# Kernel tuning notes

Measured on AMD Instinct MI355X. Metric: run time of the kernel, lower is better.

## Reference

```python
import jax, jax.numpy as jnp
import numpy as np

N, E, CIN = 50000, 400000, 512
GH, GO, TH, HEADS, COUT = 128, 64, 64, 4, 32
BN_EPS = 1e-5


def setup_inputs() -> dict:
    key = jax.random.key(0)
    ks = jax.random.split(key, 40)
    i = iter(range(40))
    nrm = lambda shape, s=0.05: jax.random.normal(ks[next(i)], shape, jnp.float32) * s
    uni = lambda shape, lo, hi: jax.random.uniform(ks[next(i)], shape, jnp.float32, lo, hi)
    inp = {
        'x': jax.random.normal(ks[next(i)], (N, CIN), jnp.float32),
        'edge_index': jax.random.randint(ks[next(i)], (2, E), 0, N, jnp.int32),
        'edge_weight': uni((E,), 0.0, 1.0),
        # GCN layer 1 + BN1 (eval-mode running stats)
        'W1': nrm((CIN, GH)), 'b1': jnp.zeros((GH,), jnp.float32),
        'g1': uni((GH,), 0.9, 1.1), 'be1': nrm((GH,)), 'm1': nrm((GH,)), 'v1': uni((GH,), 0.5, 1.5),
        # GCN layer 2 + BN2
        'W2': nrm((GH, GO)), 'b2': jnp.zeros((GO,), jnp.float32),
        'g2': uni((GO,), 0.9, 1.1), 'be2': nrm((GO,)), 'm2': nrm((GO,)), 'v2': uni((GO,), 0.5, 1.5),
        # TransformerConv (PyG): lin_q/k/v: GO -> HEADS*TH ; skip: GO -> TH
        'Wq': nrm((GO, HEADS * TH)), 'bq': jnp.zeros((HEADS * TH,), jnp.float32),
        'Wk': nrm((GO, HEADS * TH)), 'bk': jnp.zeros((HEADS * TH,), jnp.float32),
        'Wv': nrm((GO, HEADS * TH)), 'bv': jnp.zeros((HEADS * TH,), jnp.float32),
        'Wskip': nrm((GO, TH)), 'bskip': jnp.zeros((TH,), jnp.float32),
        # BN after transformer
        'gt': uni((TH,), 0.9, 1.1), 'bet': nrm((TH,)), 'mt': nrm((TH,)), 'vt': uni((TH,), 0.5, 1.5),
        # final Linear
        'Wfc': nrm((TH, COUT)), 'bfc': jnp.zeros((COUT,), jnp.float32),
    }
    return inp


def _bn_eval(h, g, b, m, v):
    return (h - m) * (g / jnp.sqrt(v + BN_EPS)) + b


def _gcn_conv(x, src, dst, w, W, b):
    # add self loops with weight 1 (PyG gcn_norm default)
    loop = jnp.arange(N, dtype=src.dtype)
    s = jnp.concatenate([src, loop])
    d = jnp.concatenate([dst, loop])
    w2 = jnp.concatenate([w, jnp.ones((N,), x.dtype)])
    deg = jax.ops.segment_sum(w2, d, num_segments=N)
    dinv = jnp.where(deg > 0, jax.lax.rsqrt(deg), 0.0)
    norm = dinv[s] * w2 * dinv[d]                      # [E+N]
    h = x @ W                                          # [N, F]
    out = jax.ops.segment_sum(norm[:, None] * h[s], d, num_segments=N)
    return out + b


def _transformer_conv(x, src, dst, Wq, bq, Wk, bk, Wv, bv, Wskip, bskip):
    # PyG TransformerConv, concat=False (mean over heads), root_weight=True, no self loops
    q = (x @ Wq + bq).reshape(N, HEADS, TH)
    k = (x @ Wk + bk).reshape(N, HEADS, TH)
    v = (x @ Wv + bv).reshape(N, HEADS, TH)
    score = jnp.einsum('ehd,ehd->eh', q[dst], k[src]) / jnp.sqrt(jnp.float32(TH))  # [E,H]
    smax = jax.ops.segment_max(score, dst, num_segments=N)       # [N,H]
    ex = jnp.exp(score - smax[dst])
    denom = jax.ops.segment_sum(ex, dst, num_segments=N)         # [N,H]
    alpha = ex / (denom[dst] + 1e-16)                            # edge softmax over incoming edges
    agg = jax.ops.segment_sum(alpha[:, :, None] * v[src], dst, num_segments=N)  # [N,H,TH]
    out = agg.mean(axis=1)                                       # concat=False -> head mean
    return out + x @ Wskip + bskip


def reference(x, edge_index, edge_weight,
              W1, b1, g1, be1, m1, v1,
              W2, b2, g2, be2, m2, v2,
              Wq, bq, Wk, bk, Wv, bv, Wskip, bskip,
              gt, bet, mt, vt, Wfc, bfc):
    src, dst = edge_index[0], edge_index[1]
    h = _gcn_conv(x, src, dst, edge_weight, W1, b1)
    h = jax.nn.relu(_bn_eval(h, g1, be1, m1, v1))        # dropout = identity in eval
    h = _gcn_conv(h, src, dst, edge_weight, W2, b2)
    z = jax.nn.relu(_bn_eval(h, g2, be2, m2, v2))
    z = _transformer_conv(z, src, dst, Wq, bq, Wk, bk, Wv, bv, Wskip, bskip)
    z = jax.nn.relu(_bn_eval(z, gt, bet, mt, vt))
    return z @ Wfc + bfc
```

## Files before the change

### kernel.cpp

```cpp
#include <hip/hip_runtime.h>
#include <math.h>

namespace {

constexpr int NN = 50000;
constexpr int EE = 400000;
constexpr int CIN = 512;
constexpr int GH = 128;
constexpr int GO = 64;
constexpr int HEADS = 4;
constexpr int COUT = 32;
constexpr float EPS = 1e-5f;
constexpr int PBLK = (NN + 255) / 256;
constexpr int EDGEB = (EE + 255) / 256;
constexpr int PREPB = 128 + (79872 + 255) / 256;
constexpr int GM = (NN + 63) / 64;

typedef __attribute__((ext_vector_type(8))) _Float16 half8;
typedef __attribute__((ext_vector_type(4))) _Float16 half4;
typedef __attribute__((ext_vector_type(2))) _Float16 half2v;
typedef __attribute__((ext_vector_type(4))) float f32x4;

inline int cdiv(int a, int b) { return (a + b - 1) / b; }

__global__ void k_init0(float* deg, int* cnt) {
  int i = blockIdx.x * blockDim.x + threadIdx.x;
  if (i < NN) { deg[i] = 0.0f; cnt[i] = 0; }
}

__device__ __forceinline__ void prep_body(
    int b, int tid,
    const float* __restrict__ Wq, const float* __restrict__ Wk,
    const float* __restrict__ bq, const float* __restrict__ Wv,
    const float* __restrict__ bv, const float* __restrict__ bsk,
    const float* __restrict__ W1, const float* __restrict__ W2,
    const float* __restrict__ Wsk, const float* __restrict__ Wfc,
    _Float16* __restrict__ Mcp, float* __restrict__ cvec,
    _Float16* __restrict__ Bcatp, float* __restrict__ bcomb,
    _Float16* __restrict__ W1p, _Float16* __restrict__ W2p,
    _Float16* __restrict__ Wfcp) {
  if (b < 64) {
    const int i = b, col = tid, h = col >> 6, j = col & 63;
    float acc = 0.f;
    for (int t = 0; t < 64; ++t)
      acc += Wq[i * 256 + h * 64 + t] * Wk[j * 256 + h * 64 + t];
    Mcp[col * 64 + i] = (_Float16)(0.125f * acc);
    if (i == 0) {
      float c = 0.f;
      for (int t = 0; t < 64; ++t) c += bq[h * 64 + t] * Wk[j * 256 + h * 64 + t];
      cvec[col] = 0.125f * c;
    }
  } else if (b < 128) {
    const int idx = (b - 64) * 256 + tid;
    const int rr = idx >> 6, t = idx & 63;
    const int h = rr >> 6, c = rr & 63;
    Bcatp[(size_t)t * 320 + 64 + rr] = (_Float16)(0.25f * Wv[c * 256 + h * 64 + t]);
    if (b == 64 && tid < 64) {
      float s = 0.f;
#pragma unroll
      for (int h2 = 0; h2 < 4; ++h2) s += bv[h2 * 64 + tid];
      bcomb[tid] = bsk[tid] + 0.25f * s;
    }
  } else {
    const int i = (b - 128) * 256 + tid;
    if (i < 65536) { int k = i >> 7, f = i & 127; W1p[f * 512 + k] = (_Float16)W1[i]; }
    else if (i < 73728) { int rel = i - 65536; int k = rel >> 6, f = rel & 63; W2p[f * 128 + k] = (_Float16)W2[rel]; }
    else if (i < 77824) { int rel = i - 73728; int k = rel >> 6, f = rel & 63; Bcatp[f * 320 + k] = (_Float16)Wsk[rel]; }
    else if (i < 79872) { int rel = i - 77824; int k = rel >> 5, f = rel & 31; Wfcp[f * 64 + k] = (_Float16)Wfc[rel]; }
  }
}

__launch_bounds__(256) __global__
void k_edgeprep(const int* __restrict__ ei, const float* __restrict__ w,
                float* __restrict__ deg, int* __restrict__ cnt,
                int* __restrict__ rank,
                const float* __restrict__ Wq, const float* __restrict__ Wk,
                const float* __restrict__ bq, const float* __restrict__ Wv,
                const float* __restrict__ bv, const float* __restrict__ bsk,
                const float* __restrict__ W1, const float* __restrict__ W2,
                const float* __restrict__ Wsk, const float* __restrict__ Wfc,
                _Float16* __restrict__ Mcp, float* __restrict__ cvec,
                _Float16* __restrict__ Bcatp, float* __restrict__ bcomb,
                _Float16* __restrict__ W1p, _Float16* __restrict__ W2p,
                _Float16* __restrict__ Wfcp) {
  if (blockIdx.x < EDGEB) {
    int e = blockIdx.x * 256 + threadIdx.x;
    if (e < EE) {
      int d = ei[EE + e];
      atomicAdd(&deg[d], w[e]);
      rank[e] = atomicAdd(&cnt[d], 1);
    }
  } else {
    prep_body(blockIdx.x - EDGEB, threadIdx.x, Wq, Wk, bq, Wv, bv, bsk,
              W1, W2, Wsk, Wfc, Mcp, cvec, Bcatp, bcomb, W1p, W2p, Wfcp);
  }
}

__global__ void k_node1(const int* __restrict__ cnt, float* __restrict__ dinv,
                        int* __restrict__ part, int* __restrict__ bsum,
                        int* __restrict__ blkhist) {
  __shared__ int wsm[4];
  __shared__ int lh[64];
  const int tid = threadIdx.x, lane = tid & 63, wv = tid >> 6;
  const int i = blockIdx.x * 256 + tid;
  if (tid < 64) lh[tid] = 0;
  __syncthreads();
  int v = (i < NN) ? cnt[i] : 0;
  if (i < NN) {
    dinv[i] = rsqrtf(dinv[i] + 1.0f);
    atomicAdd(&lh[min(v, 63)], 1);
  }
  int x = v;
#pragma unroll
  for (int s = 1; s < 64; s <<= 1) {
    int t = __shfl_up(x, s);
    if (lane >= s) x += t;
  }
  if (lane == 63) wsm[wv] = x;
  __syncthreads();
  if (tid == 0) {
    int r = 0;
#pragma unroll
    for (int j = 0; j < 4; ++j) { int t = wsm[j]; wsm[j] = r; r += t; }
    bsum[blockIdx.x] = r;
  }
  __syncthreads();
  if (i < NN) part[i] = wsm[wv] + x - v;
  if (tid < 64) blkhist[blockIdx.x * 64 + tid] = lh[tid];
}

__launch_bounds__(256) __global__
void k_small(int* __restrict__ bsum, int* __restrict__ ro,
             const int* __restrict__ blkhist, int* __restrict__ blkoff) {
  __shared__ int wsm[4];
  __shared__ int qsum[4][64];
  const int tid = threadIdx.x, lane = tid & 63, wv = tid >> 6;
  {
    int v = (tid < PBLK) ? bsum[tid] : 0;
    int x = v;
#pragma unroll
    for (int s = 1; s < 64; s <<= 1) {
      int t = __shfl_up(x, s);
      if (lane >= s) x += t;
    }
    if (lane == 63) wsm[wv] = x;
    __syncthreads();
    if (tid == 0) {
      int r = 0;
#pragma unroll
      for (int j = 0; j < 4; ++j) { int t = wsm[j]; wsm[j] = r; r += t; }
      ro[NN] = r;
    }
    __syncthreads();
    if (tid < PBLK) bsum[tid] = wsm[wv] + x - v;
  }
  const int c0 = wv * 49, c1 = c0 + 49;
  {
    int qs = 0;
    int k = c0;
    for (; k + 4 <= c1; k += 4) {
      int a = blkhist[(k + 0) * 64 + lane];
      int b = blkhist[(k + 1) * 64 + lane];
      int c = blkhist[(k + 2) * 64 + lane];
      int d = blkhist[(k + 3) * 64 + lane];
      qs += (a + b) + (c + d);
    }
    for (; k < c1; ++k) qs += blkhist[k * 64 + lane];
    qsum[wv][lane] = qs;
  }
  __syncthreads();
  int tot = qsum[0][lane] + qsum[1][lane] + qsum[2][lane] + qsum[3][lane];
  int x = tot;
#pragma unroll
  for (int s = 1; s < 64; s <<= 1) {
    int t = __shfl_up(x, s);
    if (lane >= s) x += t;
  }
  int run = x - tot;
  for (int q = 0; q < wv; ++q) run += qsum[q][lane];
  int k = c0;
  for (; k + 4 <= c1; k += 4) {
    int a = blkhist[(k + 0) * 64 + lane];
    int b = blkhist[(k + 1) * 64 + lane];
    int c = blkhist[(k + 2) * 64 + lane];
    int d = blkhist[(k + 3) * 64 + lane];
    blkoff[(k + 0) * 64 + lane] = run;
    blkoff[(k + 1) * 64 + lane] = run + a;
    blkoff[(k + 2) * 64 + lane] = run + a + b;
    blkoff[(k + 3) * 64 + lane] = run + a + b + c;
    run += (a + b) + (c + d);
  }
  for (; k < c1; ++k) {
    int c = blkhist[k * 64 + lane];
    blkoff[k * 64 + lane] = run;
    run += c;
  }
}

__global__ void k_node2(const int* __restrict__ part, const int* __restrict__ bsum,
                        int* __restrict__ ro, const int* __restrict__ cnt,
                        const int* __restrict__ blkoff, int* __restrict__ perm) {
  __shared__ int lcur[64];
  const int tid = threadIdx.x;
  const int i = blockIdx.x * 256 + tid;
  if (tid < 64) lcur[tid] = 0;
  if (i < NN) ro[i] = part[i] + bsum[i >> 8];
  __syncthreads();
  if (i < NN) {
    int b = min(cnt[i], 63);
    int r = atomicAdd(&lcur[b], 1);
    perm[blkoff[blockIdx.x * 64 + b] + r] = i;
  }
}

template <int F, int K, int LDA, bool AF32, bool OUTF32>
__device__ __forceinline__
void hgemm_body(int bid, const void* __restrict__ Av,
                const _Float16* __restrict__ Bp, const float* __restrict__ bias,
                void* __restrict__ Cv, int M) {
  constexpr int MI = 4;
  constexpr int NR = F / 64;
  constexpr int FW = F / 4;
  constexpr int NT = K / 64;

  __shared__ _Float16 Asm[(AF32 ? 2 : 1) * 64 * 64];
  _Float16* Ah = Asm;
  _Float16* Al = Asm + 64 * 64;

  const int tid = threadIdx.x;
  const int lane = tid & 63;
  const int wc = tid >> 6;
  const int l15 = lane & 15, lhi = lane >> 4;
  const int m0 = bid * 64;
  const int r = tid >> 2, ch = tid & 3;
  const int gr = min(m0 + r, M - 1);

  f32x4 acc[MI][NR];
#pragma unroll
  for (int mi = 0; mi < MI; ++mi)
#pragma unroll
    for (int ni = 0; ni < NR; ++ni) acc[mi][ni] = (f32x4)0.0f;

  float xfA[16], xfB[16];
  half8 xhA0, xhA1, xhB0, xhB1;

  auto LOADA = [&](int kk) {
    if constexpr (AF32) {
      const float4* src = reinterpret_cast<const float4*>(
          (const float*)Av + (size_t)gr * LDA + kk + ch * 16);
      float4 f0 = src[0], f1 = src[1], f2 = src[2], f3 = src[3];
      xfA[0] = f0.x; xfA[1] = f0.y; xfA[2] = f0.z; xfA[3] = f0.w;
      xfA[4] = f1.x; xfA[5] = f1.y; xfA[6] = f1.z; xfA[7] = f1.w;
      xfA[8] = f2.x; xfA[9] = f2.y; xfA[10] = f2.z; xfA[11] = f2.w;
      xfA[12] = f3.x; xfA[13] = f3.y; xfA[14] = f3.z; xfA[15] = f3.w;
    } else {
      const half8* src = reinterpret_cast<const half8*>(
          (const _Float16*)Av + (size_t)gr * LDA + kk + ch * 16);
      xhA0 = src[0];
      xhA1 = src[1];
    }
  };
  auto LOADB = [&](int kk) {
    if constexpr (AF32) {
      const float4* src = reinterpret_cast<const float4*>(
          (const float*)Av + (size_t)gr * LDA + kk + ch * 16);
      float4 f0 = src[0], f1 = src[1], f2 = src[2], f3 = src[3];
      xfB[0] = f0.x; xfB[1] = f0.y; xfB[2] = f0.z; xfB[3] = f0.w;
      xfB[4] = f1.x; xfB[5] = f1.y; xfB[6] = f1.z; xfB[7] = f1.w;
      xfB[8] = f2.x; xfB[9] = f2.y; xfB[10] = f2.z; xfB[11] = f2.w;
      xfB[12] = f3.x; xfB[13] = f3.y; xfB[14] = f3.z; xfB[15] = f3.w;
    } else {
      const half8* src = reinterpret_cast<const half8*>(
          (const _Float16*)Av + (size_t)gr * LDA + kk + ch * 16);
      xhB0 = src[0];
      xhB1 = src[1];
    }
  };

  const int sbase = r * 128 + ch * 32;
  const int ssw = (r & 7) << 4;
  auto STOREA = [&]() {
    if constexpr (AF32) {
      half8 vh0, vl0, vh1, vl1;
#pragma unroll
      for (int i = 0; i < 8; ++i) {
        _Float16 h = (_Float16)xfA[i];
        vh0[i] = h; vl0[i] = (_Float16)(xfA[i] - (float)h);
      }
#pragma unroll
      for (int i = 0; i < 8; ++i) {
        _Float16 h = (_Float16)xfA[8 + i];
        vh1[i] = h; vl1[i] = (_Float16)(xfA[8 + i] - (float)h);
      }
      *reinterpret_cast<half8*>((char*)Ah + (sbase ^ ssw)) = vh0;
      *reinterpret_cast<half8*>((char*)Ah + ((sbase + 16) ^ ssw)) = vh1;
      *reinterpret_cast<half8*>((char*)Al + (sbase ^ ssw)) = vl0;
      *reinterpret_cast<half8*>((char*)Al + ((sbase + 16) ^ ssw)) = vl1;
    } else {
      *reinterpret_cast<half8*>((char*)Ah + (sbase ^ ssw)) = xhA0;
      *reinterpret_cast<half8*>((char*)Ah + ((sbase + 16) ^ ssw)) = xhA1;
    }
  };
  auto STOREB = [&]() {
    if constexpr (AF32) {
      half8 vh0, vl0, vh1, vl1;
#pragma unroll
      for (int i = 0; i < 8; ++i) {
        _Float16 h = (_Float16)xfB[i];
        vh0[i] = h; vl0[i] = (_Float16)(xfB[i] - (float)h);
      }
#pragma unroll
      for (int i = 0; i < 8; ++i) {
        _Float16 h = (_Float16)xfB[8 + i];
        vh1[i] = h; vl1[i] = (_Float16)(xfB[8 + i] - (float)h);
      }
      *reinterpret_cast<half8*>((char*)Ah + (sbase ^ ssw)) = vh0;
      *reinterpret_cast<half8*>((char*)Ah + ((sbase + 16) ^ ssw)) = vh1;
      *reinterpret_cast<half8*>((char*)Al + (sbase ^ ssw)) = vl0;
      *reinterpret_cast<half8*>((char*)Al + ((sbase + 16) ^ ssw)) = vl1;
    } else {
      *reinterpret_cast<half8*>((char*)Ah + (sbase ^ ssw)) = xhB0;
      *reinterpret_cast<half8*>((char*)Ah + ((sbase + 16) ^ ssw)) = xhB1;
    }
  };

  LOADA(0);
  if constexpr (NT > 1) LOADB(64);

#pragma unroll
  for (int t = 0; t < NT; ++t) {
    if ((t & 1) == 0) STOREA(); else STOREB();
    __syncthreads();
    if ((t & 1) == 0) {
      if (t + 2 < NT) LOADA((t + 2) * 64);
    } else {
      if (t + 2 < NT) LOADB((t + 2) * 64);
    }
    const int k0 = t * 64;
#pragma unroll
    for (int ks = 0; ks < 2; ++ks) {
      half8 ah[MI], al[MI];
#pragma unroll
      for (int mi = 0; mi < MI; ++mi) {
        const int row = mi * 16 + l15;
        const int off = (row * 128 + (ks * 32 + lhi * 8) * 2) ^ ((row & 7) << 4);
        ah[mi] = *reinterpret_cast<const half8*>((const char*)Ah + off);
        if constexpr (AF32)
          al[mi] = *reinterpret_cast<const half8*>((const char*)Al + off);
      }
#pragma unroll
      for (int ni = 0; ni < NR; ++ni) {
        const int col = wc * FW + ni * 16 + l15;
        const half8 bf = *reinterpret_cast<const half8*>(
            Bp + (size_t)col * K + k0 + ks * 32 + lhi * 8);
#pragma unroll
        for (int mi = 0; mi < MI; ++mi) {
          acc[mi][ni] = __builtin_amdgcn_mfma_f32_16x16x32_f16(ah[mi], bf, acc[mi][ni], 0, 0, 0);
          if constexpr (AF32)
            acc[mi][ni] = __builtin_amdgcn_mfma_f32_16x16x32_f16(al[mi], bf, acc[mi][ni], 0, 0, 0);
        }
      }
    }
    __syncthreads();
  }

#pragma unroll
  for (int ni = 0; ni < NR; ++ni) {
    const int col = wc * FW + ni * 16 + l15;
    const float bvv = bias ? bias[col] : 0.0f;
#pragma unroll
    for (int mi = 0; mi < MI; ++mi) {
#pragma unroll
      for (int rr = 0; rr < 4; ++rr) {
        const int orow = m0 + mi * 16 + lhi * 4 + rr;
        if (orow < M) {
          float val = acc[mi][ni][rr] + bvv;
          if (OUTF32)
            ((float*)Cv)[(size_t)orow * F + col] = val;
          else
            ((_Float16*)Cv)[(size_t)orow * F + col] = (_Float16)val;
        }
      }
    }
  }
}

template <int F, int K, int LDA, bool AF32, bool OUTF32>
__launch_bounds__(256) __global__
void hgemm(const void* __restrict__ Av, const _Float16* __restrict__ Bp,
           const float* __restrict__ bias, void* __restrict__ Cv, int M) {
  hgemm_body<F, K, LDA, AF32, OUTF32>(blockIdx.x, Av, Bp, bias, Cv, M);
}

__launch_bounds__(256) __global__
void k_fillgemm1(const int* __restrict__ ei, const float* __restrict__ w,
                 const float* __restrict__ dinv, const int* __restrict__ ro,
                 const int* __restrict__ rank, int* __restrict__ csr_src,
                 float* __restrict__ csr_nrm, const float* __restrict__ x,
                 const _Float16* __restrict__ W1p, _Float16* __restrict__ h1f,
                 int M) {
  if (blockIdx.x < GM) {
    hgemm_body<128, 512, 512, true, false>(blockIdx.x, x, W1p, nullptr, h1f, M);
  } else {
    int e = (blockIdx.x - GM) * 256 + threadIdx.x;
    if (e < EE) {
      int s = ei[e], d = ei[EE + e];
      int p = ro[d] + rank[e];
      csr_src[p] = s;
      csr_nrm[p] = dinv[s] * w[e] * dinv[d];
    }
  }
}

__launch_bounds__(256) __global__
void k_aggfc(const _Float16* __restrict__ zu, const _Float16* __restrict__ Bcatp,
             const float* __restrict__ bcomb, const _Float16* __restrict__ Wfcp,
             const float* __restrict__ bfc, float* __restrict__ out, int M,
             const float* __restrict__ gt, const float* __restrict__ bet,
             const float* __restrict__ mt, const float* __restrict__ vt) {
  __shared__ _Float16 Ah[64 * 64];
  __shared__ _Float16 Gs[64 * 64];

  const int tid = threadIdx.x;
  const int lane = tid & 63;
  const int wid = tid >> 6;
  const int l15 = lane & 15, lhi = lane >> 4;
  const int m0 = blockIdx.x * 64;
  const int r = tid >> 2, ch = tid & 3;
  const int gr = min(m0 + r, M - 1);

  f32x4 acc[4];
#pragma unroll
  for (int mi = 0; mi < 4; ++mi) acc[mi] = (f32x4)0.0f;

  half8 xhA0, xhA1, xhB0, xhB1;
  auto LOADA = [&](int kk) {
    const half8* src = reinterpret_cast<const half8*>(
        zu + (size_t)gr * 320 + kk + ch * 16);
    xhA0 = src[0]; xhA1 = src[1];
  };
  auto LOADB = [&](int kk) {
    const half8* src = reinterpret_cast<const half8*>(
        zu + (size_t)gr * 320 + kk + ch * 16);
    xhB0 = src[0]; xhB1 = src[1];
  };
  const int sbase = r * 128 + ch * 32;
  const int ssw = (r & 7) << 4;
  auto STOREA = [&]() {
    *reinterpret_cast<half8*>((char*)Ah + (sbase ^ ssw)) = xhA0;
    *reinterpret_cast<half8*>((char*)Ah + ((sbase + 16) ^ ssw)) = xhA1;
  };
  auto STOREB = [&]() {
    *reinterpret_cast<half8*>((char*)Ah + (sbase ^ ssw)) = xhB0;
    *reinterpret_cast<half8*>((char*)Ah + ((sbase + 16) ^ ssw)) = xhB1;
  };

  LOADA(0);
  LOADB(64);
#pragma unroll
  for (int t = 0; t < 5; ++t) {
    if ((t & 1) == 0) STOREA(); else STOREB();
    __syncthreads();
    if ((t & 1) == 0) {
      if (t + 2 < 5) LOADA((t + 2) * 64);
    } else {
      if (t + 2 < 5) LOADB((t + 2) * 64);
    }
    const int k0 = t * 64;
#pragma unroll
    for (int ks = 0; ks < 2; ++ks) {
      half8 ah[4];
#pragma unroll
      for (int mi = 0; mi < 4; ++mi) {
        const int row = mi * 16 + l15;
        const int off = (row * 128 + (ks * 32 + lhi * 8) * 2) ^ ((row & 7) << 4);
        ah[mi] = *reinterpret_cast<const half8*>((const char*)Ah + off);
      }
      const int col = wid * 16 + l15;
      const half8 bf = *reinterpret_cast<const half8*>(
          Bcatp + (size_t)col * 320 + k0 + ks * 32 + lhi * 8);
#pragma unroll
      for (int mi = 0; mi < 4; ++mi)
        acc[mi] = __builtin_amdgcn_mfma_f32_16x16x32_f16(ah[mi], bf, acc[mi], 0, 0, 0);
    }
    __syncthreads();
  }

  {
    const int col = wid * 16 + l15;
    const float bns = gt[col] * rsqrtf(vt[col] + EPS);
    const float bnb = bet[col], bnm = mt[col], bco = bcomb[col];
#pragma unroll
    for (int mi = 0; mi < 4; ++mi) {
#pragma unroll
      for (int rr = 0; rr < 4; ++rr) {
        const int row = mi * 16 + lhi * 4 + rr;
        float val = acc[mi][rr] + bco;
        val = (val - bnm) * bns + bnb;
        val = val > 0.f ? val : 0.f;
        const int boff = (row * 128 + col * 2) ^ ((row & 7) << 4);
        *reinterpret_cast<_Float16*>((char*)Gs + boff) = (_Float16)val;
      }
    }
  }
  __syncthreads();

  f32x4 acc2[2];
#pragma unroll
  for (int ni = 0; ni < 2; ++ni) acc2[ni] = (f32x4)0.0f;
#pragma unroll
  for (int ks = 0; ks < 2; ++ks) {
    const int row = wid * 16 + l15;
    const int off = (row * 128 + (ks * 32 + lhi * 8) * 2) ^ ((row & 7) << 4);
    const half8 ag = *reinterpret_cast<const half8*>((const char*)Gs + off);
#pragma unroll
    for (int ni = 0; ni < 2; ++ni) {
      const int col = ni * 16 + l15;
      const half8 bf = *reinterpret_cast<const half8*>(
          Wfcp + (size_t)col * 64 + ks * 32 + lhi * 8);
      acc2[ni] = __builtin_amdgcn_mfma_f32_16x16x32_f16(ag, bf, acc2[ni], 0, 0, 0);
    }
  }
#pragma unroll
  for (int ni = 0; ni < 2; ++ni) {
    const int col = ni * 16 + l15;
#pragma unroll
    for (int rr = 0; rr < 4; ++rr) {
      const int orow = m0 + wid * 16 + lhi * 4 + rr;
      if (orow < M) out[(size_t)orow * COUT + col] = acc2[ni][rr] + bfc[col];
    }
  }
}

__launch_bounds__(256) __global__
void k_gcn128(const int* __restrict__ ro, const int* __restrict__ csr_src,
              const float* __restrict__ csr_nrm, const int* __restrict__ perm,
              const _Float16* __restrict__ h, const float* __restrict__ dinv,
              const float* __restrict__ bias, const float* __restrict__ g,
              const float* __restrict__ be, const float* __restrict__ m,
              const float* __restrict__ v, _Float16* __restrict__ out) {
  const int idx = blockIdx.x * 4 + (threadIdx.x >> 6);
  const int lane = threadIdx.x & 63;
  if (idx >= NN) return;
  const int wid = perm[idx];
  const float di = dinv[wid];
  const float di2 = di * di;
  const int p0 = ro[wid], p1 = ro[wid + 1];

  half2v sv = *reinterpret_cast<const half2v*>(h + (size_t)wid * 128 + lane * 2);
  float2 a[4];
  a[0] = make_float2((float)sv[0] * di2, (float)sv[1] * di2);
  a[1] = make_float2(0.f, 0.f);
  a[2] = make_float2(0.f, 0.f);
  a[3] = make_float2(0.f, 0.f);
  int p = p0;
  for (; p + 8 <= p1; p += 8) {
    int s[8]; float w[8];
#pragma unroll
    for (int j = 0; j < 8; ++j) { s[j] = csr_src[p + j]; w[j] = csr_nrm[p + j]; }
    half2v hv[8];
#pragma unroll
    for (int j = 0; j < 8; ++j)
      hv[j] = *reinterpret_cast<const half2v*>(h + (size_t)s[j] * 128 + lane * 2);
#pragma unroll
    for (int j = 0; j < 8; ++j) {
      a[j & 3].x += w[j] * (float)hv[j][0];
      a[j & 3].y += w[j] * (float)hv[j][1];
    }
  }
  for (; p + 4 <= p1; p += 4) {
    int s[4]; float w[4];
#pragma unroll
    for (int j = 0; j < 4; ++j) { s[j] = csr_src[p + j]; w[j] = csr_nrm[p + j]; }
    half2v hv[4];
#pragma unroll
    for (int j = 0; j < 4; ++j)
      hv[j] = *reinterpret_cast<const half2v*>(h + (size_t)s[j] * 128 + lane * 2);
#pragma unroll
    for (int j = 0; j < 4; ++j) {
      a[j].x += w[j] * (float)hv[j][0];
      a[j].y += w[j] * (float)hv[j][1];
    }
  }
  for (; p < p1; ++p) {
    int s = csr_src[p];
    float w = csr_nrm[p];
    half2v hv = *reinterpret_cast<const half2v*>(h + (size_t)s * 128 + lane * 2);
    a[1].x += w * (float)hv[0]; a[1].y += w * (float)hv[1];
  }
  float ax = (a[0].x + a[1].x) + (a[2].x + a[3].x);
  float ay = (a[0].y + a[1].y) + (a[2].y + a[3].y);
  float2 gg = reinterpret_cast<const float2*>(g)[lane];
  float2 bb = reinterpret_cast<const float2*>(be)[lane];
  float2 mm = reinterpret_cast<const float2*>(m)[lane];
  float2 vv = reinterpret_cast<const float2*>(v)[lane];
  float2 bi = reinterpret_cast<const float2*>(bias)[lane];
  float s0 = gg.x * rsqrtf(vv.x + EPS);
  float s1 = gg.y * rsqrtf(vv.y + EPS);
  float y0 = (ax + bi.x - mm.x) * s0 + bb.x;
  float y1 = (ay + bi.y - mm.y) * s1 + bb.y;
  half2v o;
  o[0] = (_Float16)(y0 > 0.f ? y0 : 0.f);
  o[1] = (_Float16)(y1 > 0.f ? y1 : 0.f);
  *reinterpret_cast<half2v*>(out + (size_t)wid * 128 + lane * 2) = o;
}

__launch_bounds__(256) __global__
void k_gcn64(const int* __restrict__ ro, const int* __restrict__ csr_src,
             const float* __restrict__ csr_nrm, const int* __restrict__ perm,
             const _Float16* __restrict__ h, const float* __restrict__ dinv,
             const float* __restrict__ bias, const float* __restrict__ g,
             const float* __restrict__ be, const float* __restrict__ m,
             const float* __restrict__ v, _Float16* __restrict__ zu) {
  const int idx = blockIdx.x * 4 + (threadIdx.x >> 6);
  const int lane = threadIdx.x & 63;
  if (idx >= NN) return;
  const int wid = perm[idx];
  const float di = dinv[wid];
  const float di2 = di * di;
  const int p0 = ro[wid], p1 = ro[wid + 1];

  float a[4];
  a[0] = (float)h[(size_t)wid * 64 + lane] * di2;
  a[1] = 0.f; a[2] = 0.f; a[3] = 0.f;
  int p = p0;
  for (; p + 8 <= p1; p += 8) {
    int s[8]; float w[8];
#pragma unroll
    for (int j = 0; j < 8; ++j) { s[j] = csr_src[p + j]; w[j] = csr_nrm[p + j]; }
    float hv[8];
#pragma unroll
    for (int j = 0; j < 8; ++j) hv[j] = (float)h[(size_t)s[j] * 64 + lane];
#pragma unroll
    for (int j = 0; j < 8; ++j) a[j & 3] += w[j] * hv[j];
  }
  for (; p + 4 <= p1; p += 4) {
    int s[4]; float w[4];
#pragma unroll
    for (int j = 0; j < 4; ++j) { s[j] = csr_src[p + j]; w[j] = csr_nrm[p + j]; }
    float hv[4];
#pragma unroll
    for (int j = 0; j < 4; ++j) hv[j] = (float)h[(size_t)s[j] * 64 + lane];
#pragma unroll
    for (int j = 0; j < 4; ++j) a[j] += w[j] * hv[j];
  }
  for (; p < p1; ++p) a[1] += csr_nrm[p] * (float)h[(size_t)csr_src[p] * 64 + lane];
  float av = (a[0] + a[1]) + (a[2] + a[3]);
  float sc = g[lane] * rsqrtf(v[lane] + EPS);
  float y = (av + bias[lane] - m[lane]) * sc + be[lane];
  zu[(size_t)wid * 320 + lane] = (_Float16)(y > 0.f ? y : 0.f);
}

__launch_bounds__(256) __global__
void k_attn(const int* __restrict__ ro, const int* __restrict__ csr_src,
            const int* __restrict__ perm, _Float16* zu,
            const _Float16* __restrict__ qpp) {
  const int wave = blockIdx.x * 4 + (threadIdx.x >> 6);
  const int lane = threadIdx.x & 63;
  const int g = lane >> 4;
  const int t = lane & 15;
  const bool bit3 = (t & 8) != 0, bit2 = (t & 4) != 0;

  const int idx = wave * 4 + g;
  const bool valid = idx < NN;
  const int dst = perm[valid ? idx : 0];

  float4 q[4];
#pragma unroll
  for (int h = 0; h < 4; ++h) {
    half4 qh = *reinterpret_cast<const half4*>(qpp + (size_t)dst * 256 + h * 64 + t * 4);
    q[h] = make_float4((float)qh[0], (float)qh[1], (float)qh[2], (float)qh[3]);
  }

  float4 ua[4];
  float den[4];
#pragma unroll
  for (int h = 0; h < 4; ++h) {
    ua[h] = make_float4(0.f, 0.f, 0.f, 0.f);
    den[h] = 0.f;
  }

  int p = valid ? ro[dst] : 0;
  const int pend = valid ? ro[dst + 1] : 0;

  auto reduce4 = [&](float pa0, float pa1, float pa2, float pa3,
                     float& o0, float& o1, float& o2, float& o3) {
    float send1 = bit3 ? pa0 : pa2;
    float recv1 = __shfl_xor(send1, 8);
    float a0 = (bit3 ? pa2 : pa0) + recv1;
    float send2 = bit3 ? pa1 : pa3;
    float recv2 = __shfl_xor(send2, 8);
    float a1 = (bit3 ? pa3 : pa1) + recv2;
    float send3 = bit2 ? a0 : a1;
    float recv3 = __shfl_xor(send3, 4);
    float b = (bit2 ? a1 : a0) + recv3;
    b += __shfl_xor(b, 2);
    b += __shfl_xor(b, 1);
    float r4 = __shfl_xor(b, 4);
    float r8 = __shfl_xor(b, 8);
    float r84 = __shfl_xor(r4, 8);
    o0 = bit3 ? (bit2 ? r84 : r8) : (bit2 ? r4 : b);
    o1 = bit3 ? (bit2 ? r8 : r84) : (bit2 ? b : r4);
    o2 = bit3 ? (bit2 ? r4 : b) : (bit2 ? r84 : r8);
    o3 = bit3 ? (bit2 ? b : r4) : (bit2 ? r8 : r84);
  };

  int sA = csr_src[min(p, EE - 1)];
  int sB = csr_src[min(p + 1, EE - 1)];
  half4 znA = *reinterpret_cast<const half4*>(zu + (size_t)sA * 320 + t * 4);
  half4 znB = *reinterpret_cast<const half4*>(zu + (size_t)sB * 320 + t * 4);

  while (__ballot(p < pend)) {
    const bool actA = p < pend;
    const bool actB = (p + 1) < pend;
    const float4 zvA = make_float4((float)znA[0], (float)znA[1], (float)znA[2], (float)znA[3]);
    const float4 zvB = make_float4((float)znB[0], (float)znB[1], (float)znB[2], (float)znB[3]);
    sA = csr_src[min(p + 2, EE - 1)];
    sB = csr_src[min(p + 3, EE - 1)];
    znA = *reinterpret_cast<const half4*>(zu + (size_t)sA * 320 + t * 4);
    znB = *reinterpret_cast<const half4*>(zu + (size_t)sB * 320 + t * 4);

    float pA0 = q[0].x * zvA.x + q[0].y * zvA.y + q[0].z * zvA.z + q[0].w * zvA.w;
    float pA1 = q[1].x * zvA.x + q[1].y * zvA.y + q[1].z * zvA.z + q[1].w * zvA.w;
    float pA2 = q[2].x * zvA.x + q[2].y * zvA.y + q[2].z * zvA.z + q[2].w * zvA.w;
    float pA3 = q[3].x * zvA.x + q[3].y * zvA.y + q[3].z * zvA.z + q[3].w * zvA.w;
    float pB0 = q[0].x * zvB.x + q[0].y * zvB.y + q[0].z * zvB.z + q[0].w * zvB.w;
    float pB1 = q[1].x * zvB.x + q[1].y * zvB.y + q[1].z * zvB.z + q[1].w * zvB.w;
    float pB2 = q[2].x * zvB.x + q[2].y * zvB.y + q[2].z * zvB.z + q[2].w * zvB.w;
    float pB3 = q[3].x * zvB.x + q[3].y * zvB.y + q[3].z * zvB.z + q[3].w * zvB.w;

    float sA0, sA1, sA2, sA3, sB0, sB1, sB2, sB3;
    reduce4(pA0, pA1, pA2, pA3, sA0, sA1, sA2, sA3);
    reduce4(pB0, pB1, pB2, pB3, sB0, sB1, sB2, sB3);

    float eA0 = actA ? __expf(fminf(sA0, 60.f)) : 0.f;
    float eA1 = actA ? __expf(fminf(sA1, 60.f)) : 0.f;
    float eA2 = actA ? __expf(fminf(sA2, 60.f)) : 0.f;
    float eA3 = actA ? __expf(fminf(sA3, 60.f)) : 0.f;
    float eB0 = actB ? __expf(fminf(sB0, 60.f)) : 0.f;
    float eB1 = actB ? __expf(fminf(sB1, 60.f)) : 0.f;
    float eB2 = actB ? __expf(fminf(sB2, 60.f)) : 0.f;
    float eB3 = actB ? __expf(fminf(sB3, 60.f)) : 0.f;

    den[0] += eA0 + eB0; den[1] += eA1 + eB1;
    den[2] += eA2 + eB2; den[3] += eA3 + eB3;
    ua[0].x += eA0 * zvA.x + eB0 * zvB.x; ua[0].y += eA0 * zvA.y + eB0 * zvB.y;
    ua[0].z += eA0 * zvA.z + eB0 * zvB.z; ua[0].w += eA0 * zvA.w + eB0 * zvB.w;
    ua[1].x += eA1 * zvA.x + eB1 * zvB.x; ua[1].y += eA1 * zvA.y + eB1 * zvB.y;
    ua[1].z += eA1 * zvA.z + eB1 * zvB.z; ua[1].w += eA1 * zvA.w + eB1 * zvB.w;
    ua[2].x += eA2 * zvA.x + eB2 * zvB.x; ua[2].y += eA2 * zvA.y + eB2 * zvB.y;
    ua[2].z += eA2 * zvA.z + eB2 * zvB.z; ua[2].w += eA2 * zvA.w + eB2 * zvB.w;
    ua[3].x += eA3 * zvA.x + eB3 * zvB.x; ua[3].y += eA3 * zvA.y + eB3 * zvB.y;
    ua[3].z += eA3 * zvA.z + eB3 * zvB.z; ua[3].w += eA3 * zvA.w + eB3 * zvB.w;
    p += 2;
  }

  if (valid) {
#pragma unroll
    for (int h = 0; h < 4; ++h) {
      float inv = 1.0f / (den[h] + 1e-16f);
      half4 o;
      o[0] = (_Float16)(ua[h].x * inv);
      o[1] = (_Float16)(ua[h].y * inv);
      o[2] = (_Float16)(ua[h].z * inv);
      o[3] = (_Float16)(ua[h].w * inv);
      *reinterpret_cast<half4*>(zu + (size_t)dst * 320 + 64 + h * 64 + t * 4) = o;
    }
  }
}

}

extern "C" void kernel_launch(void* const* d_in, const int* in_sizes, int n_in,
                              void* d_out, int out_size, void* d_ws, size_t ws_size,
                              hipStream_t stream) {
  const float* x   = (const float*)d_in[0];
  const int*   ei  = (const int*)d_in[1];
  const float* ew  = (const float*)d_in[2];
  const float* W1  = (const float*)d_in[3];
  const float* b1  = (const float*)d_in[4];
  const float* g1  = (const float*)d_in[5];
  const float* be1 = (const float*)d_in[6];
  const float* m1  = (const float*)d_in[7];
  const float* v1  = (const float*)d_in[8];
  const float* W2  = (const float*)d_in[9];
  const float* b2  = (const float*)d_in[10];
  const float* g2  = (const float*)d_in[11];
  const float* be2 = (const float*)d_in[12];
  const float* m2  = (const float*)d_in[13];
  const float* v2  = (const float*)d_in[14];
  const float* Wq  = (const float*)d_in[15];
  const float* bq  = (const float*)d_in[16];
  const float* Wk  = (const float*)d_in[17];
  const float* Wv  = (const float*)d_in[19];
  const float* bv  = (const float*)d_in[20];
  const float* Wsk = (const float*)d_in[21];
  const float* bsk = (const float*)d_in[22];
  const float* gt  = (const float*)d_in[23];
  const float* bet = (const float*)d_in[24];
  const float* mt  = (const float*)d_in[25];
  const float* vt  = (const float*)d_in[26];
  const float* Wfc = (const float*)d_in[27];
  const float* bfc = (const float*)d_in[28];

  constexpr int NP = 50048;
  float* ws = (float*)d_ws;
  float* dinv    = ws;
  int*   cnt     = (int*)(dinv + NP);
  int*   rank    = cnt + NP;
  int*   ro      = rank + EE;
  int*   perm    = ro + NP;
  int*   part    = perm + NP;
  int*   bsum    = part + NP;
  int*   csr_src = bsum + 256;
  float* csr_nrm = (float*)(csr_src + EE);
  int*   blkhist = (int*)(csr_nrm + EE);
  int*   blkoff  = blkhist + PBLK * 64;
  float* cvec    = (float*)(blkoff + PBLK * 64 + 64);
  float* bcomb   = cvec + 256;
  _Float16* Mcp   = (_Float16*)(bcomb + 64);
  _Float16* Bcatp = Mcp + 256 * 64;
  _Float16* W1p   = Bcatp + 64 * 320;
  _Float16* W2p   = W1p + 128 * 512;
  _Float16* Wfcp  = W2p + 64 * 128;
  _Float16* h1f   = Wfcp + 32 * 64;
  _Float16* a1f   = h1f + (size_t)NP * 128;
  _Float16* h2f   = a1f + (size_t)NP * 128;
  _Float16* zuf   = h2f + (size_t)NP * 64;
  _Float16* qppf  = zuf + (size_t)NP * 320;

  const int tb = 256;

  k_init0<<<cdiv(NN, tb), tb, 0, stream>>>(dinv, cnt);
  k_edgeprep<<<EDGEB + PREPB, 256, 0, stream>>>(
      ei, ew, dinv, cnt, rank, Wq, Wk, bq, Wv, bv, bsk, W1, W2, Wsk, Wfc,
      Mcp, cvec, Bcatp, bcomb, W1p, W2p, Wfcp);
  k_node1<<<PBLK, 256, 0, stream>>>(cnt, dinv, part, bsum, blkhist);
  k_small<<<1, 256, 0, stream>>>(bsum, ro, blkhist, blkoff);
  k_node2<<<PBLK, 256, 0, stream>>>(part, bsum, ro, cnt, blkoff, perm);

  k_fillgemm1<<<GM + EDGEB, 256, 0, stream>>>(ei, ew, dinv, ro, rank, csr_src,
                                              csr_nrm, x, W1p, h1f, NN);

  k_gcn128<<<cdiv(NN, 4), 256, 0, stream>>>(ro, csr_src, csr_nrm, perm, h1f, dinv,
                                            b1, g1, be1, m1, v1, a1f);
  hgemm<64, 128, 128, false, false><<<GM, 256, 0, stream>>>(a1f, W2p, nullptr, h2f, NN);
  k_gcn64<<<cdiv(NN, 4), 256, 0, stream>>>(ro, csr_src, csr_nrm, perm, h2f, dinv,
                                           b2, g2, be2, m2, v2, zuf);

  hgemm<256, 64, 320, false, false><<<GM, 256, 0, stream>>>(zuf, Mcp, cvec, qppf, NN);
  k_attn<<<cdiv(NN, 16), 256, 0, stream>>>(ro, csr_src, perm, zuf, qppf);

  k_aggfc<<<GM, 256, 0, stream>>>(zuf, Bcatp, bcomb, Wfcp, bfc, (float*)d_out, NN,
                                  gt, bet, mt, vt);
}
```

Measured before the change: 228.5 us.

## Pre-convert x to fp16 and drop split-precision GEMM1; pack CSR src/norm

Adds a conversion pass in the edge-prep kernel that writes x as fp16. The first GEMM can then use single-pass fp16 MFMA instead of hi/lo split-fp16 emulation, which halves its MFMA count and its LDS traffic. Separately, the CSR source index and normalisation weight are packed into one int2 array, so the gather kernels issue one load per edge instead of two. The trade-off is an extra read and write of x (about 150 MB of traffic), lower precision on the first layer's input, and more bytes read in the attention kernel, which only needs the index.

```diff
diff --git a/kernel.cpp b/kernel.cpp
--- a/kernel.cpp
+++ b/kernel.cpp
@@ -13,6 +13,7 @@
 constexpr float EPS = 1e-5f;
 constexpr int PBLK = (NN + 255) / 256;
 constexpr int EDGEB = (EE + 255) / 256;
+constexpr int CVTB = (NN * CIN) / 2048;
 constexpr int PREPB = 128 + (79872 + 255) / 256;
 constexpr int GM = (NN + 63) / 64;
 
@@ -73,7 +74,8 @@
 __launch_bounds__(256) __global__
 void k_edgeprep(const int* __restrict__ ei, const float* __restrict__ w,
                 float* __restrict__ deg, int* __restrict__ cnt,
-                int* __restrict__ rank,
+                int* __restrict__ rank, const float* __restrict__ x,
+                _Float16* __restrict__ x16,
                 const float* __restrict__ Wq, const float* __restrict__ Wk,
                 const float* __restrict__ bq, const float* __restrict__ Wv,
                 const float* __restrict__ bv, const float* __restrict__ bsk,
@@ -90,8 +92,18 @@
       atomicAdd(&deg[d], w[e]);
       rank[e] = atomicAdd(&cnt[d], 1);
     }
+  } else if (blockIdx.x < EDGEB + CVTB) {
+    const int base = (blockIdx.x - EDGEB) * 2048 + threadIdx.x * 8;
+    const float4 f0 = *reinterpret_cast<const float4*>(x + base);
+    const float4 f1 = *reinterpret_cast<const float4*>(x + base + 4);
+    half8 o;
+    o[0] = (_Float16)f0.x; o[1] = (_Float16)f0.y;
+    o[2] = (_Float16)f0.z; o[3] = (_Float16)f0.w;
+    o[4] = (_Float16)f1.x; o[5] = (_Float16)f1.y;
+    o[6] = (_Float16)f1.z; o[7] = (_Float16)f1.w;
+    *reinterpret_cast<half8*>(x16 + base) = o;
   } else {
-    prep_body(blockIdx.x - EDGEB, threadIdx.x, Wq, Wk, bq, Wv, bv, bsk,
+    prep_body(blockIdx.x - EDGEB - CVTB, threadIdx.x, Wq, Wk, bq, Wv, bv, bsk,
               W1, W2, Wsk, Wfc, Mcp, cvec, Bcatp, bcomb, W1p, W2p, Wfcp);
   }
 }
@@ -213,9 +225,9 @@
   }
 }
 
-template <int F, int K, int LDA, bool AF32, bool OUTF32>
+template <int F, int K, int LDA, bool OUTF32>
 __device__ __forceinline__
-void hgemm_body(int bid, const void* __restrict__ Av,
+void hgemm_body(int bid, const _Float16* __restrict__ Av,
                 const _Float16* __restrict__ Bp, const float* __restrict__ bias,
                 void* __restrict__ Cv, int M) {
   constexpr int MI = 4;
@@ -223,9 +235,7 @@
   constexpr int FW = F / 4;
   constexpr int NT = K / 64;
 
-  __shared__ _Float16 Asm[(AF32 ? 2 : 1) * 64 * 64];
-  _Float16* Ah = Asm;
-  _Float16* Al = Asm + 64 * 64;
+  __shared__ _Float16 Ah[64 * 64];
 
   const int tid = threadIdx.x;
   const int lane = tid & 63;
@@ -241,87 +251,26 @@
 #pragma unroll
     for (int ni = 0; ni < NR; ++ni) acc[mi][ni] = (f32x4)0.0f;
 
-  float xfA[16], xfB[16];
   half8 xhA0, xhA1, xhB0, xhB1;
-
   auto LOADA = [&](int kk) {
-    if constexpr (AF32) {
-      const float4* src = reinterpret_cast<const float4*>(
-          (const float*)Av + (size_t)gr * LDA + kk + ch * 16);
-      float4 f0 = src[0], f1 = src[1], f2 = src[2], f3 = src[3];
-      xfA[0] = f0.x; xfA[1] = f0.y; xfA[2] = f0.z; xfA[3] = f0.w;
-      xfA[4] = f1.x; xfA[5] = f1.y; xfA[6] = f1.z; xfA[7] = f1.w;
-      xfA[8] = f2.x; xfA[9] = f2.y; xfA[10] = f2.z; xfA[11] = f2.w;
-      xfA[12] = f3.x; xfA[13] = f3.y; xfA[14] = f3.z; xfA[15] = f3.w;
-    } else {
-      const half8* src = reinterpret_cast<const half8*>(
-          (const _Float16*)Av + (size_t)gr * LDA + kk + ch * 16);
-      xhA0 = src[0];
-      xhA1 = src[1];
-    }
+    const half8* src = reinterpret_cast<const half8*>(
+        Av + (size_t)gr * LDA + kk + ch * 16);
+    xhA0 = src[0]; xhA1 = src[1];
   };
   auto LOADB = [&](int kk) {
-    if constexpr (AF32) {
-      const float4* src = reinterpret_cast<const float4*>(
-          (const float*)Av + (size_t)gr * LDA + kk + ch * 16);
-      float4 f0 = src[0], f1 = src[1], f2 = src[2], f3 = src[3];
-      xfB[0] = f0.x; xfB[1] = f0.y; xfB[2] = f0.z; xfB[3] = f0.w;
-      xfB[4] = f1.x; xfB[5] = f1.y; xfB[6] = f1.z; xfB[7] = f1.w;
-      xfB[8] = f2.x; xfB[9] = f2.y; xfB[10] = f2.z; xfB[11] = f2.w;
-      xfB[12] = f3.x; xfB[13] = f3.y; xfB[14] = f3.z; xfB[15] = f3.w;
-    } else {
-      const half8* src = reinterpret_cast<const half8*>(
-          (const _Float16*)Av + (size_t)gr * LDA + kk + ch * 16);
-      xhB0 = src[0];
-      xhB1 = src[1];
-    }
+    const half8* src = reinterpret_cast<const half8*>(
+        Av + (size_t)gr * LDA + kk + ch * 16);
+    xhB0 = src[0]; xhB1 = src[1];
   };
-
   const int sbase = r * 128 + ch * 32;
   const int ssw = (r & 7) << 4;
   auto STOREA = [&]() {
-    if constexpr (AF32) {
-      half8 vh0, vl0, vh1, vl1;
-#pragma unroll
-      for (int i = 0; i < 8; ++i) {
-        _Float16 h = (_Float16)xfA[i];
-        vh0[i] = h; vl0[i] = (_Float16)(xfA[i] - (float)h);
-      }
-#pragma unroll
-      for (int i = 0; i < 8; ++i) {
-        _Float16 h = (_Float16)xfA[8 + i];
-        vh1[i] = h; vl1[i] = (_Float16)(xfA[8 + i] - (float)h);
-      }
-      *reinterpret_cast<half8*>((char*)Ah + (sbase ^ ssw)) = vh0;
-      *reinterpret_cast<half8*>((char*)Ah + ((sbase + 16) ^ ssw)) = vh1;
-      *reinterpret_cast<half8*>((char*)Al + (sbase ^ ssw)) = vl0;
-      *reinterpret_cast<half8*>((char*)Al + ((sbase + 16) ^ ssw)) = vl1;
-    } else {
-      *reinterpret_cast<half8*>((char*)Ah + (sbase ^ ssw)) = xhA0;
-      *reinterpret_cast<half8*>((char*)Ah + ((sbase + 16) ^ ssw)) = xhA1;
-    }
+    *reinterpret_cast<half8*>((char*)Ah + (sbase ^ ssw)) = xhA0;
+    *reinterpret_cast<half8*>((char*)Ah + ((sbase + 16) ^ ssw)) = xhA1;
   };
   auto STOREB = [&]() {
-    if constexpr (AF32) {
-      half8 vh0, vl0, vh1, vl1;
-#pragma unroll
-      for (int i = 0; i < 8; ++i) {
-        _Float16 h = (_Float16)xfB[i];
-        vh0[i] = h; vl0[i] = (_Float16)(xfB[i] - (float)h);
-      }
-#pragma unroll
-      for (int i = 0; i < 8; ++i) {
-        _Float16 h = (_Float16)xfB[8 + i];
-        vh1[i] = h; vl1[i] = (_Float16)(xfB[8 + i] - (float)h);
-      }
-      *reinterpret_cast<half8*>((char*)Ah + (sbase ^ ssw)) = vh0;
-      *reinterpret_cast<half8*>((char*)Ah + ((sbase + 16) ^ ssw)) = vh1;
-      *reinterpret_cast<half8*>((char*)Al + (sbase ^ ssw)) = vl0;
-      *reinterpret_cast<half8*>((char*)Al + ((sbase + 16) ^ ssw)) = vl1;
-    } else {
-      *reinterpret_cast<half8*>((char*)Ah + (sbase ^ ssw)) = xhB0;
-      *reinterpret_cast<half8*>((char*)Ah + ((sbase + 16) ^ ssw)) = xhB1;
-    }
+    *reinterpret_cast<half8*>((char*)Ah + (sbase ^ ssw)) = xhB0;
+    *reinterpret_cast<half8*>((char*)Ah + ((sbase + 16) ^ ssw)) = xhB1;
   };
 
   LOADA(0);
@@ -339,14 +288,12 @@
     const int k0 = t * 64;
 #pragma unroll
     for (int ks = 0; ks < 2; ++ks) {
-      half8 ah[MI], al[MI];
+      half8 ah[MI];
 #pragma unroll
       for (int mi = 0; mi < MI; ++mi) {
         const int row = mi * 16 + l15;
         const int off = (row * 128 + (ks * 32 + lhi * 8) * 2) ^ ((row & 7) << 4);
         ah[mi] = *reinterpret_cast<const half8*>((const char*)Ah + off);
-        if constexpr (AF32)
-          al[mi] = *reinterpret_cast<const half8*>((const char*)Al + off);
       }
 #pragma unroll
       for (int ni = 0; ni < NR; ++ni) {
@@ -354,11 +301,8 @@
         const half8 bf = *reinterpret_cast<const half8*>(
             Bp + (size_t)col * K + k0 + ks * 32 + lhi * 8);
 #pragma unroll
-        for (int mi = 0; mi < MI; ++mi) {
+        for (int mi = 0; mi < MI; ++mi)
           acc[mi][ni] = __builtin_amdgcn_mfma_f32_16x16x32_f16(ah[mi], bf, acc[mi][ni], 0, 0, 0);
-          if constexpr (AF32)
-            acc[mi][ni] = __builtin_amdgcn_mfma_f32_16x16x32_f16(al[mi], bf, acc[mi][ni], 0, 0, 0);
-        }
       }
     }
     __syncthreads();
@@ -385,29 +329,31 @@
   }
 }
 
-template <int F, int K, int LDA, bool AF32, bool OUTF32>
+template <int F, int K, int LDA, bool OUTF32>
 __launch_bounds__(256) __global__
-void hgemm(const void* __restrict__ Av, const _Float16* __restrict__ Bp,
+void hgemm(const _Float16* __restrict__ Av, const _Float16* __restrict__ Bp,
            const float* __restrict__ bias, void* __restrict__ Cv, int M) {
-  hgemm_body<F, K, LDA, AF32, OUTF32>(blockIdx.x, Av, Bp, bias, Cv, M);
+  hgemm_body<F, K, LDA, OUTF32>(blockIdx.x, Av, Bp, bias, Cv, M);
 }
 
 __launch_bounds__(256) __global__
 void k_fillgemm1(const int* __restrict__ ei, const float* __restrict__ w,
                  const float* __restrict__ dinv, const int* __restrict__ ro,
-                 const int* __restrict__ rank, int* __restrict__ csr_src,
-                 float* __restrict__ csr_nrm, const float* __restrict__ x,
+                 const int* __restrict__ rank, int2* __restrict__ csrp,
+                 const _Float16* __restrict__ x16,
                  const _Float16* __restrict__ W1p, _Float16* __restrict__ h1f,
                  int M) {
   if (blockIdx.x < GM) {
-    hgemm_body<128, 512, 512, true, false>(blockIdx.x, x, W1p, nullptr, h1f, M);
+    hgemm_body<128, 512, 512, false>(blockIdx.x, x16, W1p, nullptr, h1f, M);
   } else {
     int e = (blockIdx.x - GM) * 256 + threadIdx.x;
     if (e < EE) {
       int s = ei[e], d = ei[EE + e];
       int p = ro[d] + rank[e];
-      csr_src[p] = s;
-      csr_nrm[p] = dinv[s] * w[e] * dinv[d];
+      int2 pk;
+      pk.x = s;
+      pk.y = __float_as_int(dinv[s] * w[e] * dinv[d]);
+      csrp[p] = pk;
     }
   }
 }
@@ -533,8 +479,8 @@
 }
 
 __launch_bounds__(256) __global__
-void k_gcn128(const int* __restrict__ ro, const int* __restrict__ csr_src,
-              const float* __restrict__ csr_nrm, const int* __restrict__ perm,
+void k_gcn128(const int* __restrict__ ro, const int2* __restrict__ csrp,
+              const int* __restrict__ perm,
               const _Float16* __restrict__ h, const float* __restrict__ dinv,
               const float* __restrict__ bias, const float* __restrict__ g,
               const float* __restrict__ be, const float* __restrict__ m,
@@ -555,37 +501,39 @@
   a[3] = make_float2(0.f, 0.f);
   int p = p0;
   for (; p + 8 <= p1; p += 8) {
-    int s[8]; float w[8];
-#pragma unroll
-    for (int j = 0; j < 8; ++j) { s[j] = csr_src[p + j]; w[j] = csr_nrm[p + j]; }
+    int2 pk[8];
+#pragma unroll
+    for (int j = 0; j < 8; ++j) pk[j] = csrp[p + j];
     half2v hv[8];
 #pragma unroll
     for (int j = 0; j < 8; ++j)
-      hv[j] = *reinterpret_cast<const half2v*>(h + (size_t)s[j] * 128 + lane * 2);
+      hv[j] = *reinterpret_cast<const half2v*>(h + (size_t)pk[j].x * 128 + lane * 2);
 #pragma unroll
     for (int j = 0; j < 8; ++j) {
-      a[j & 3].x += w[j] * (float)hv[j][0];
-      a[j & 3].y += w[j] * (float)hv[j][1];
+      float w = __int_as_float(pk[j].y);
+      a[j & 3].x += w * (float)hv[j][0];
+      a[j & 3].y += w * (float)hv[j][1];
     }
   }
   for (; p + 4 <= p1; p += 4) {
-    int s[4]; float w[4];
-#pragma unroll
-    for (int j = 0; j < 4; ++j) { s[j] = csr_src[p + j]; w[j] = csr_nrm[p + j]; }
+    int2 pk[4];
+#pragma unroll
+    for (int j = 0; j < 4; ++j) pk[j] = csrp[p + j];
     half2v hv[4];
 #pragma unroll
     for (int j = 0; j < 4; ++j)
-      hv[j] = *reinterpret_cast<const half2v*>(h + (size_t)s[j] * 128 + lane * 2);
+      hv[j] = *reinterpret_cast<const half2v*>(h + (size_t)pk[j].x * 128 + lane * 2);
 #pragma unroll
     for (int j = 0; j < 4; ++j) {
-      a[j].x += w[j] * (float)hv[j][0];
-      a[j].y += w[j] * (float)hv[j][1];
+      float w = __int_as_float(pk[j].y);
+      a[j].x += w * (float)hv[j][0];
+      a[j].y += w * (float)hv[j][1];
     }
   }
   for (; p < p1; ++p) {
-    int s = csr_src[p];
-    float w = csr_nrm[p];
-    half2v hv = *reinterpret_cast<const half2v*>(h + (size_t)s * 128 + lane * 2);
+    int2 pk = csrp[p];
+    float w = __int_as_float(pk.y);
+    half2v hv = *reinterpret_cast<const half2v*>(h + (size_t)pk.x * 128 + lane * 2);
     a[1].x += w * (float)hv[0]; a[1].y += w * (float)hv[1];
   }
   float ax = (a[0].x + a[1].x) + (a[2].x + a[3].x);
@@ -606,8 +554,8 @@
 }
 
 __launch_bounds__(256) __global__
-void k_gcn64(const int* __restrict__ ro, const int* __restrict__ csr_src,
-             const float* __restrict__ csr_nrm, const int* __restrict__ perm,
+void k_gcn64(const int* __restrict__ ro, const int2* __restrict__ csrp,
+             const int* __restrict__ perm,
              const _Float16* __restrict__ h, const float* __restrict__ dinv,
              const float* __restrict__ bias, const float* __restrict__ g,
              const float* __restrict__ be, const float* __restrict__ m,
@@ -625,26 +573,29 @@
   a[1] = 0.f; a[2] = 0.f; a[3] = 0.f;
   int p = p0;
   for (; p + 8 <= p1; p += 8) {
-    int s[8]; float w[8];
-#pragma unroll
-    for (int j = 0; j < 8; ++j) { s[j] = csr_src[p + j]; w[j] = csr_nrm[p + j]; }
+    int2 pk[8];
+#pragma unroll
+    for (int j = 0; j < 8; ++j) pk[j] = csrp[p + j];
     float hv[8];
 #pragma unroll
-    for (int j = 0; j < 8; ++j) hv[j] = (float)h[(size_t)s[j] * 64 + lane];
-#pragma unroll
-    for (int j = 0; j < 8; ++j) a[j & 3] += w[j] * hv[j];
+    for (int j = 0; j < 8; ++j) hv[j] = (float)h[(size_t)pk[j].x * 64 + lane];
+#pragma unroll
+    for (int j = 0; j < 8; ++j) a[j & 3] += __int_as_float(pk[j].y) * hv[j];
   }
   for (; p + 4 <= p1; p += 4) {
-    int s[4]; float w[4];
-#pragma unroll
-    for (int j = 0; j < 4; ++j) { s[j] = csr_src[p + j]; w[j] = csr_nrm[p + j]; }
+    int2 pk[4];
+#pragma unroll
+    for (int j = 0; j < 4; ++j) pk[j] = csrp[p + j];
     float hv[4];
 #pragma unroll
-    for (int j = 0; j < 4; ++j) hv[j] = (float)h[(size_t)s[j] * 64 + lane];
-#pragma unroll
-    for (int j = 0; j < 4; ++j) a[j] += w[j] * hv[j];
-  }
-  for (; p < p1; ++p) a[1] += csr_nrm[p] * (float)h[(size_t)csr_src[p] * 64 + lane];
+    for (int j = 0; j < 4; ++j) hv[j] = (float)h[(size_t)pk[j].x * 64 + lane];
+#pragma unroll
+    for (int j = 0; j < 4; ++j) a[j] += __int_as_float(pk[j].y) * hv[j];
+  }
+  for (; p < p1; ++p) {
+    int2 pk = csrp[p];
+    a[1] += __int_as_float(pk.y) * (float)h[(size_t)pk.x * 64 + lane];
+  }
   float av = (a[0] + a[1]) + (a[2] + a[3]);
   float sc = g[lane] * rsqrtf(v[lane] + EPS);
   float y = (av + bias[lane] - m[lane]) * sc + be[lane];
@@ -652,7 +603,7 @@
 }
 
 __launch_bounds__(256) __global__
-void k_attn(const int* __restrict__ ro, const int* __restrict__ csr_src,
+void k_attn(const int* __restrict__ ro, const int2* __restrict__ csrp,
             const int* __restrict__ perm, _Float16* zu,
             const _Float16* __restrict__ qpp) {
   const int wave = blockIdx.x * 4 + (threadIdx.x >> 6);
@@ -705,8 +656,8 @@
     o3 = bit3 ? (bit2 ? b : r4) : (bit2 ? r8 : r84);
   };
 
-  int sA = csr_src[min(p, EE - 1)];
-  int sB = csr_src[min(p + 1, EE - 1)];
+  int sA = csrp[min(p, EE - 1)].x;
+  int sB = csrp[min(p + 1, EE - 1)].x;
   half4 znA = *reinterpret_cast<const half4*>(zu + (size_t)sA * 320 + t * 4);
   half4 znB = *reinterpret_cast<const half4*>(zu + (size_t)sB * 320 + t * 4);
 
@@ -715,8 +666,8 @@
     const bool actB = (p + 1) < pend;
     const float4 zvA = make_float4((float)znA[0], (float)znA[1], (float)znA[2], (float)znA[3]);
     const float4 zvB = make_float4((float)znB[0], (float)znB[1], (float)znB[2], (float)znB[3]);
-    sA = csr_src[min(p + 2, EE - 1)];
-    sB = csr_src[min(p + 3, EE - 1)];
+    sA = csrp[min(p + 2, EE - 1)].x;
+    sB = csrp[min(p + 3, EE - 1)].x;
     znA = *reinterpret_cast<const half4*>(zu + (size_t)sA * 320 + t * 4);
     znB = *reinterpret_cast<const half4*>(zu + (size_t)sB * 320 + t * 4);
 
@@ -812,9 +763,8 @@
   int*   perm    = ro + NP;
   int*   part    = perm + NP;
   int*   bsum    = part + NP;
-  int*   csr_src = bsum + 256;
-  float* csr_nrm = (float*)(csr_src + EE);
-  int*   blkhist = (int*)(csr_nrm + EE);
+  int2*  csrp    = (int2*)(bsum + 256);
+  int*   blkhist = (int*)(csrp + EE);
   int*   blkoff  = blkhist + PBLK * 64;
   float* cvec    = (float*)(blkoff + PBLK * 64 + 64);
   float* bcomb   = cvec + 256;
@@ -823,7 +773,8 @@
   _Float16* W1p   = Bcatp + 64 * 320;
   _Float16* W2p   = W1p + 128 * 512;
   _Float16* Wfcp  = W2p + 64 * 128;
-  _Float16* h1f   = Wfcp + 32 * 64;
+  _Float16* x16   = Wfcp + 32 * 64;
+  _Float16* h1f   = x16 + (size_t)NP * 512;
   _Float16* a1f   = h1f + (size_t)NP * 128;
   _Float16* h2f   = a1f + (size_t)NP * 128;
   _Float16* zuf   = h2f + (size_t)NP * 64;
@@ -832,24 +783,24 @@
   const int tb = 256;
 
   k_init0<<<cdiv(NN, tb), tb, 0, stream>>>(dinv, cnt);
-  k_edgeprep<<<EDGEB + PREPB, 256, 0, stream>>>(
-      ei, ew, dinv, cnt, rank, Wq, Wk, bq, Wv, bv, bsk, W1, W2, Wsk, Wfc,
+  k_edgeprep<<<EDGEB + CVTB + PREPB, 256, 0, stream>>>(
+      ei, ew, dinv, cnt, rank, x, x16, Wq, Wk, bq, Wv, bv, bsk, W1, W2, Wsk, Wfc,
       Mcp, cvec, Bcatp, bcomb, W1p, W2p, Wfcp);
   k_node1<<<PBLK, 256, 0, stream>>>(cnt, dinv, part, bsum, blkhist);
   k_small<<<1, 256, 0, stream>>>(bsum, ro, blkhist, blkoff);
   k_node2<<<PBLK, 256, 0, stream>>>(part, bsum, ro, cnt, blkoff, perm);
 
-  k_fillgemm1<<<GM + EDGEB, 256, 0, stream>>>(ei, ew, dinv, ro, rank, csr_src,
-                                              csr_nrm, x, W1p, h1f, NN);
-
-  k_gcn128<<<cdiv(NN, 4), 256, 0, stream>>>(ro, csr_src, csr_nrm, perm, h1f, dinv,
+  k_fillgemm1<<<GM + EDGEB, 256, 0, stream>>>(ei, ew, dinv, ro, rank, csrp,
+                                              x16, W1p, h1f, NN);
+
+  k_gcn128<<<cdiv(NN, 4), 256, 0, stream>>>(ro, csrp, perm, h1f, dinv,
                                             b1, g1, be1, m1, v1, a1f);
-  hgemm<64, 128, 128, false, false><<<GM, 256, 0, stream>>>(a1f, W2p, nullptr, h2f, NN);
-  k_gcn64<<<cdiv(NN, 4), 256, 0, stream>>>(ro, csr_src, csr_nrm, perm, h2f, dinv,
+  hgemm<64, 128, 128, false><<<GM, 256, 0, stream>>>(a1f, W2p, nullptr, h2f, NN);
+  k_gcn64<<<cdiv(NN, 4), 256, 0, stream>>>(ro, csrp, perm, h2f, dinv,
                                            b2, g2, be2, m2, v2, zuf);
 
-  hgemm<256, 64, 320, false, false><<<GM, 256, 0, stream>>>(zuf, Mcp, cvec, qppf, NN);
-  k_attn<<<cdiv(NN, 16), 256, 0, stream>>>(ro, csr_src, perm, zuf, qppf);
+  hgemm<256, 64, 320, false><<<GM, 256, 0, stream>>>(zuf, Mcp, cvec, qppf, NN);
+  k_attn<<<cdiv(NN, 16), 256, 0, stream>>>(ro, csrp, perm, zuf, qppf);
 
   k_aggfc<<<GM, 256, 0, stream>>>(zuf, Bcatp, bcomb, Wfcp, bfc, (float*)d_out, NN,
                                   gt, bet, mt, vt);
```

Measured after the change: 239.3 us. +4.7%, slower.
